# Kernel tuning notes

Measured on AMD Instinct MI355X. Metric: run time of the kernel, lower is better.

Reference implementation:

```python
import jax, jax.numpy as jnp
import numpy as np

B, S, E, H = 2, 2048, 1024, 16
D = E // H  # head_dim = 64

def setup_inputs() -> dict:
    key = jax.random.key(0)
    ks = jax.random.split(key, 9)
    scale = 1.0 / np.sqrt(E)
    inp = {"x": jax.random.normal(ks[0], (B, S, E), dtype=jnp.float32)}
    for i, name in enumerate(["q", "k", "v", "o"]):
        inp[f"W{name}"] = jax.random.uniform(ks[1 + 2 * i], (E, E), jnp.float32, -scale, scale)
        inp[f"b{name}"] = jax.random.uniform(ks[2 + 2 * i], (E,), jnp.float32, -scale, scale)
    return inp

def reference(x, Wq, bq, Wk, bk, Wv, bv, Wo, bo):
    b, s, e = x.shape
    q = x @ Wq + bq
    k = x @ Wk + bk
    v = x @ Wv + bv
    # Faithful to source: view(B, H, S, D) with NO transpose -> splits the
    # sequence dimension across heads (each head sees a contiguous chunk of
    # s*d elements reinterpreted as [s, d]).
    q = q.reshape(b, H, s, D)
    k = k.reshape(b, H, s, D)
    v = v.reshape(b, H, s, D)
    scores = jnp.einsum("bhqd,bhkd->bhqk", q, k) / np.sqrt(D)
    # mask=False in source still adds a zeros mask (no-op); omitted.
    probs = jax.nn.softmax(scores, axis=-1)
    xhat = jnp.einsum("bhqk,bhkd->bhqd", probs, v)
    # transpose(1, 2).contiguous().view(B, S, E)
    xhat = xhat.transpose(0, 2, 1, 3).reshape(b, s, e)
    return xhat @ Wo + bo
```

## Files before the change

kernel.cpp:

```cpp
#include <hip/hip_runtime.h>
#include <math.h>

#define B_ 2
#define S_ 2048
#define E_ 1024
#define H_ 16
#define D_ 64

typedef __attribute__((ext_vector_type(8))) short short8;
typedef __attribute__((ext_vector_type(4))) float f32x4;
typedef __attribute__((ext_vector_type(4))) unsigned short us4;
typedef __attribute__((ext_vector_type(8))) unsigned short us8;
typedef unsigned short ushort_t;

#define MFMA16 __builtin_amdgcn_mfma_f32_16x16x32_bf16

__device__ __forceinline__ ushort_t f2bf(float f) {
    unsigned int u = __float_as_uint(f);
    u += 0x7FFFu + ((u >> 16) & 1u);
    return (ushort_t)(u >> 16);
}
__device__ __forceinline__ float bf2f(ushort_t h) {
    return __uint_as_float((unsigned int)h << 16);
}

__device__ __forceinline__ void gload16(const void* g, void* l) {
    __builtin_amdgcn_global_load_lds(
        (__attribute__((address_space(1))) void*)(unsigned long long)g,
        (__attribute__((address_space(3))) void*)(unsigned int)(unsigned long long)l,
        16, 0, 0);
}

__global__ __launch_bounds__(256)
void split_x(const float* __restrict__ in, ushort_t* __restrict__ hi)
{
    const size_t base = ((size_t)blockIdx.x * 256 + threadIdx.x) * 8;
    float v[8];
    *reinterpret_cast<float4*>(&v[0]) = *reinterpret_cast<const float4*>(&in[base]);
    *reinterpret_cast<float4*>(&v[4]) = *reinterpret_cast<const float4*>(&in[base + 4]);
    us8 h;
#pragma unroll
    for (int j = 0; j < 8; ++j) h[j] = f2bf(v[j]);
    *reinterpret_cast<us8*>(&hi[base]) = h;
}

__global__ __launch_bounds__(256)
void wsplit_t(const float* __restrict__ Wq, const float* __restrict__ Wk,
              const float* __restrict__ Wv, const float* __restrict__ Wo,
              ushort_t* __restrict__ Wth, ushort_t* __restrict__ Wtl)
{
    __shared__ float T[64][65];
    const int tid = threadIdx.x;
    const int z = blockIdx.z;
    const float* W = (z == 0) ? Wq : (z == 1) ? Wk : (z == 2) ? Wv : Wo;
    const int kt = blockIdx.y * 64;
    const int nt = blockIdx.x * 64;

    const int lr = (tid >> 4) * 4;
    const int lc = (tid & 15) * 4;
#pragma unroll
    for (int i = 0; i < 4; ++i) {
        float4 v = *reinterpret_cast<const float4*>(&W[(size_t)(kt + lr + i) * 1024 + nt + lc]);
        T[lr + i][lc + 0] = v.x; T[lr + i][lc + 1] = v.y;
        T[lr + i][lc + 2] = v.z; T[lr + i][lc + 3] = v.w;
    }
    __syncthreads();

    const int n = tid >> 2;
    const int kc = (tid & 3) * 16;
    us8 h[2], l[2];
#pragma unroll
    for (int u = 0; u < 2; ++u)
#pragma unroll
        for (int j = 0; j < 8; ++j) {
            float v = T[kc + u * 8 + j][n];
            ushort_t hh = f2bf(v);
            h[u][j] = hh;
            l[u][j] = f2bf(v - bf2f(hh));
        }
    ushort_t* dh = Wth + ((size_t)z * 1024 + nt + n) * 1024 + kt + kc;
    ushort_t* dl = Wtl + ((size_t)z * 1024 + nt + n) * 1024 + kt + kc;
    *reinterpret_cast<us8*>(dh)     = h[0];
    *reinterpret_cast<us8*>(dh + 8) = h[1];
    *reinterpret_cast<us8*>(dl)     = l[0];
    *reinterpret_cast<us8*>(dl + 8) = l[1];
}

__global__ __launch_bounds__(256, 3)
void gemm_qkv(const ushort_t* __restrict__ xh, const ushort_t* __restrict__ Wth,
              const float* __restrict__ bq, const float* __restrict__ bk,
              const float* __restrict__ bv,
              ushort_t* __restrict__ Qb, ushort_t* __restrict__ Kb,
              ushort_t* __restrict__ Vb, float qalpha)
{
    __shared__ ushort_t As[128 * 32], Bs[128 * 32];
    const int which = blockIdx.x >> 3;
    const int n0 = (blockIdx.x & 7) * 128;
    const int m0 = blockIdx.y * 128;
    const ushort_t* Bh = Wth + (size_t)which * 1024 * 1024;
    const float* bias = (which == 0) ? bq : (which == 1) ? bk : bv;
    ushort_t* out = (which == 0) ? Qb : (which == 1) ? Kb : Vb;
    const float alpha = (which == 0) ? qalpha : 1.0f;

    const int tid  = threadIdx.x;
    const int lane = tid & 63;
    const int w    = tid >> 6;
    const int l15  = lane & 15;
    const int g    = lane >> 4;
    const int wr   = w >> 1;
    const int wc   = w & 1;

    const int sr  = lane >> 2;
    const int scz = (lane & 3) ^ ((sr >> 1) & 3);
    const int sc  = scz * 8;
    const int j0 = w * 2, j1 = j0 + 1;

    const ushort_t* gA0 = xh + (size_t)(m0 + j0 * 16 + sr) * 1024 + sc;
    const ushort_t* gA1 = xh + (size_t)(m0 + j1 * 16 + sr) * 1024 + sc;
    const ushort_t* gB0 = Bh + (size_t)(n0 + j0 * 16 + sr) * 1024 + sc;
    const ushort_t* gB1 = Bh + (size_t)(n0 + j1 * 16 + sr) * 1024 + sc;

    const int sx  = (l15 >> 1) & 3;
    const int rd1 = (((g >> 1) + 0) ^ sx) * 8 + (g & 1) * 4;
    const int rd2 = (((g >> 1) + 2) ^ sx) * 8 + (g & 1) * 4;

    f32x4 acc[4][4];
#pragma unroll
    for (int i = 0; i < 4; ++i)
#pragma unroll
        for (int j = 0; j < 4; ++j) { acc[i][j][0] = 0.f; acc[i][j][1] = 0.f; acc[i][j][2] = 0.f; acc[i][j][3] = 0.f; }

    for (int kt = 0; kt < 32; ++kt) {
        const int k0 = kt * 32;
        if (kt) __syncthreads();
        gload16(gA0 + k0, As + j0 * 512);
        gload16(gA1 + k0, As + j1 * 512);
        gload16(gB0 + k0, Bs + j0 * 512);
        gload16(gB1 + k0, Bs + j1 * 512);
        asm volatile("s_waitcnt vmcnt(0)" ::: "memory");
        __syncthreads();

        short8 bh[4];
#pragma unroll
        for (int nb = 0; nb < 4; ++nb) {
            const int rb = (wc * 64 + nb * 16 + l15) * 32;
            union { us4 h[2]; short8 s; } u;
            u.h[0] = *reinterpret_cast<const us4*>(Bs + rb + rd1);
            u.h[1] = *reinterpret_cast<const us4*>(Bs + rb + rd2);
            bh[nb] = u.s;
        }
#pragma unroll
        for (int mb = 0; mb < 4; ++mb) {
            const int rb = (wr * 64 + mb * 16 + l15) * 32;
            union { us4 h[2]; short8 s; } ua;
            ua.h[0] = *reinterpret_cast<const us4*>(As + rb + rd1);
            ua.h[1] = *reinterpret_cast<const us4*>(As + rb + rd2);
            const short8 ah = ua.s;
#pragma unroll
            for (int nb = 0; nb < 4; ++nb)
                acc[mb][nb] = MFMA16(ah, bh[nb], acc[mb][nb], 0, 0, 0);
        }
    }

    float bvv[4];
#pragma unroll
    for (int nb = 0; nb < 4; ++nb) bvv[nb] = bias[n0 + wc * 64 + nb * 16 + l15];
#pragma unroll
    for (int mb = 0; mb < 4; ++mb)
#pragma unroll
        for (int r = 0; r < 4; ++r) {
            const size_t row = m0 + wr * 64 + mb * 16 + 4 * g + r;
#pragma unroll
            for (int nb = 0; nb < 4; ++nb) {
                const float vv = (acc[mb][nb][r] + bvv[nb]) * alpha;
                out[row * 1024 + n0 + wc * 64 + nb * 16 + l15] = f2bf(vv);
            }
        }
}

__global__ __launch_bounds__(256, 2)
void gemm_o64(const ushort_t* __restrict__ Ah, const ushort_t* __restrict__ Al,
              const ushort_t* __restrict__ Bh, const ushort_t* __restrict__ Bl,
              const float* __restrict__ bias, float* __restrict__ out)
{
    __shared__ ushort_t AsH[128 * 32], AsL[128 * 32], BsH[64 * 32], BsL[64 * 32];
    const int tid  = threadIdx.x;
    const int lane = tid & 63;
    const int w    = tid >> 6;
    const int l15  = lane & 15;
    const int g    = lane >> 4;
    const int wr   = w >> 1;
    const int wc   = w & 1;
    const int n0 = blockIdx.x * 64;
    const int m0 = blockIdx.y * 128;

    const int sr  = lane >> 2;
    const int scz = (lane & 3) ^ ((sr >> 1) & 3);
    const int sc  = scz * 8;
    const int ja0 = 2 * w, ja1 = 2 * w + 1;

    const ushort_t* gAh0 = Ah + (size_t)(m0 + ja0 * 16 + sr) * 1024 + sc;
    const ushort_t* gAh1 = Ah + (size_t)(m0 + ja1 * 16 + sr) * 1024 + sc;
    const ushort_t* gAl0 = Al + (size_t)(m0 + ja0 * 16 + sr) * 1024 + sc;
    const ushort_t* gAl1 = Al + (size_t)(m0 + ja1 * 16 + sr) * 1024 + sc;
    const ushort_t* gBh0 = Bh + (size_t)(n0 + w * 16 + sr) * 1024 + sc;
    const ushort_t* gBl0 = Bl + (size_t)(n0 + w * 16 + sr) * 1024 + sc;

    const int sx  = (l15 >> 1) & 3;
    const int rd1 = (((g >> 1) + 0) ^ sx) * 8 + (g & 1) * 4;
    const int rd2 = (((g >> 1) + 2) ^ sx) * 8 + (g & 1) * 4;

    f32x4 acc[4][2];
#pragma unroll
    for (int i = 0; i < 4; ++i)
#pragma unroll
        for (int j = 0; j < 2; ++j) { acc[i][j][0] = 0.f; acc[i][j][1] = 0.f; acc[i][j][2] = 0.f; acc[i][j][3] = 0.f; }

    for (int kt = 0; kt < 32; ++kt) {
        const int k0 = kt * 32;
        if (kt) __syncthreads();
        gload16(gAh0 + k0, AsH + ja0 * 512);
        gload16(gAh1 + k0, AsH + ja1 * 512);
        gload16(gAl0 + k0, AsL + ja0 * 512);
        gload16(gAl1 + k0, AsL + ja1 * 512);
        gload16(gBh0 + k0, BsH + w * 512);
        gload16(gBl0 + k0, BsL + w * 512);
        asm volatile("s_waitcnt vmcnt(0)" ::: "memory");
        __syncthreads();

        short8 bh[2], bl[2];
#pragma unroll
        for (int nb = 0; nb < 2; ++nb) {
            const int rb = (wc * 32 + nb * 16 + l15) * 32;
            union { us4 h[2]; short8 s; } u;
            u.h[0] = *reinterpret_cast<const us4*>(BsH + rb + rd1);
            u.h[1] = *reinterpret_cast<const us4*>(BsH + rb + rd2);
            bh[nb] = u.s;
            union { us4 h[2]; short8 s; } v;
            v.h[0] = *reinterpret_cast<const us4*>(BsL + rb + rd1);
            v.h[1] = *reinterpret_cast<const us4*>(BsL + rb + rd2);
            bl[nb] = v.s;
        }
#pragma unroll
        for (int mb = 0; mb < 4; ++mb) {
            const int rb = (wr * 64 + mb * 16 + l15) * 32;
            union { us4 h[2]; short8 s; } ua;
            ua.h[0] = *reinterpret_cast<const us4*>(AsH + rb + rd1);
            ua.h[1] = *reinterpret_cast<const us4*>(AsH + rb + rd2);
            union { us4 h[2]; short8 s; } ul;
            ul.h[0] = *reinterpret_cast<const us4*>(AsL + rb + rd1);
            ul.h[1] = *reinterpret_cast<const us4*>(AsL + rb + rd2);
            const short8 ah = ua.s, al = ul.s;
#pragma unroll
            for (int nb = 0; nb < 2; ++nb) {
                acc[mb][nb] = MFMA16(ah, bh[nb], acc[mb][nb], 0, 0, 0);
                acc[mb][nb] = MFMA16(al, bh[nb], acc[mb][nb], 0, 0, 0);
                acc[mb][nb] = MFMA16(ah, bl[nb], acc[mb][nb], 0, 0, 0);
            }
        }
    }

    float bvv[2];
#pragma unroll
    for (int nb = 0; nb < 2; ++nb) bvv[nb] = bias[n0 + wc * 32 + nb * 16 + l15];
#pragma unroll
    for (int mb = 0; mb < 4; ++mb)
#pragma unroll
        for (int r = 0; r < 4; ++r) {
            const size_t row = m0 + wr * 64 + mb * 16 + 4 * g + r;
#pragma unroll
            for (int nb = 0; nb < 2; ++nb)
                out[row * 1024 + n0 + wc * 32 + nb * 16 + l15] = acc[mb][nb][r] + bvv[nb];
        }
}

__global__ __launch_bounds__(256, 2)
void attn_mfma(const ushort_t* __restrict__ Q, const ushort_t* __restrict__ K,
               const ushort_t* __restrict__ V, ushort_t* __restrict__ XHh,
               ushort_t* __restrict__ XHl)
{
    __shared__ __align__(16) ushort_t Kf[4 * 2 * 64 * 8];
    __shared__ __align__(16) ushort_t Vf[4 * 2 * 64 * 8];

    const int tid  = threadIdx.x;
    const int w    = tid >> 6;
    const int lane = tid & 63;
    const int l15  = lane & 15;
    const int g    = lane >> 4;

    const int qb = blockIdx.x;
    const int bh = blockIdx.y;
    const int b  = bh >> 4;
    const int hh = bh & 15;
    const size_t hoff = (size_t)b * S_ * E_ + (size_t)hh * S_ * D_;
    const ushort_t* Qh = Q + hoff;
    const ushort_t* Kh = K + hoff;
    const ushort_t* Vh = V + hoff;

    const int qw = qb * 128 + w * 32;

    short8 qf[2][2];
#pragma unroll
    for (int qg = 0; qg < 2; ++qg)
#pragma unroll
        for (int m = 0; m < 2; ++m) {
            const ushort_t* src = &Qh[(size_t)(qw + 16 * qg + l15) * D_ + 32 * m + 4 * g];
            us4 lo = *reinterpret_cast<const us4*>(src);
            us4 hi = *reinterpret_cast<const us4*>(src + 16);
            union { us4 h[2]; short8 s; } u;
            u.h[0] = lo; u.h[1] = hi;
            qf[qg][m] = u.s;
        }

    const int kr  = tid >> 2;
    const int kc0 = tid & 3;
    const int kkc = tid >> 4;
    const int vdc = tid & 15;
    const int vmc = kkc >> 3;
    const int vh  = (kkc >> 2) & 1;
    const int vg  = kkc & 3;
    const int vn  = vdc >> 2;

    f32x4 o[2][4];
#pragma unroll
    for (int qg = 0; qg < 2; ++qg)
#pragma unroll
        for (int n = 0; n < 4; ++n)
#pragma unroll
            for (int r = 0; r < 4; ++r) o[qg][n][r] = 0.f;

    float mrun[2] = {-1e30f, -1e30f};
    float lrun[2] = {0.f, 0.f};

    for (int kt = 0; kt < S_ / 64; ++kt) {
        us8 kreg[2];
#pragma unroll
        for (int u = 0; u < 2; ++u) {
            const int c8 = kc0 + 4 * u;
            kreg[u] = *reinterpret_cast<const us8*>(&Kh[(size_t)(kt * 64 + kr) * D_ + 8 * c8]);
        }
        us4 vreg[4];
#pragma unroll
        for (int i = 0; i < 4; ++i)
            vreg[i] = *reinterpret_cast<const us4*>(&Vh[(size_t)(kt * 64 + 4 * kkc + i) * D_ + 4 * vdc]);

        __syncthreads();

#pragma unroll
        for (int u = 0; u < 2; ++u) {
            const int c8 = kc0 + 4 * u;
            const int m = c8 >> 2;
            const int h = (c8 >> 1) & 1;
#pragma unroll
            for (int jh = 0; jh < 2; ++jh) {
                const int gk = (2 * c8 + jh) & 3;
                const int slot = gk * 16 + (kr & 15);
                us4 val;
#pragma unroll
                for (int i = 0; i < 4; ++i) val[i] = (ushort_t)kreg[u][4 * jh + i];
                *reinterpret_cast<us4*>(&Kf[((((kr >> 4) * 2 + m) * 64 + slot) * 8) + h * 4]) = val;
            }
        }
#pragma unroll
        for (int jj = 0; jj < 4; ++jj) {
            us4 val;
#pragma unroll
            for (int i = 0; i < 4; ++i) val[i] = vreg[i][jj];
            const int slot = vg * 16 + 4 * (vdc & 3) + jj;
            *reinterpret_cast<us4*>(&Vf[(((vn * 2 + vmc) * 64 + slot) * 8) + vh * 4]) = val;
        }
        __syncthreads();

        short8 kf[4][2];
#pragma unroll
        for (int kkb = 0; kkb < 4; ++kkb)
#pragma unroll
            for (int m = 0; m < 2; ++m)
                kf[kkb][m] = *reinterpret_cast<const short8*>(&Kf[((kkb * 2 + m) * 64 + lane) * 8]);

        f32x4 s[2][4];
#pragma unroll
        for (int qg = 0; qg < 2; ++qg)
#pragma unroll
            for (int kkb = 0; kkb < 4; ++kkb) {
                f32x4 z; z[0] = 0.f; z[1] = 0.f; z[2] = 0.f; z[3] = 0.f;
                z = MFMA16(kf[kkb][0], qf[qg][0], z, 0, 0, 0);
                s[qg][kkb] = MFMA16(kf[kkb][1], qf[qg][1], z, 0, 0, 0);
            }

        short8 vf[4][2];
#pragma unroll
        for (int n = 0; n < 4; ++n)
#pragma unroll
            for (int m = 0; m < 2; ++m)
                vf[n][m] = *reinterpret_cast<const short8*>(&Vf[((n * 2 + m) * 64 + lane) * 8]);

#pragma unroll
        for (int qg = 0; qg < 2; ++qg) {
            float t = s[qg][0][0];
#pragma unroll
            for (int kkb = 0; kkb < 4; ++kkb)
#pragma unroll
                for (int r = 0; r < 4; ++r) t = fmaxf(t, s[qg][kkb][r]);
            t = fmaxf(t, __shfl_xor(t, 16));
            t = fmaxf(t, __shfl_xor(t, 32));
            const float mnew = fmaxf(mrun[qg], t);
            const float corr = __builtin_amdgcn_exp2f(mrun[qg] - mnew);

            float rs = 0.f;
#pragma unroll
            for (int kkb = 0; kkb < 4; ++kkb)
#pragma unroll
                for (int r = 0; r < 4; ++r) {
                    const float p = __builtin_amdgcn_exp2f(s[qg][kkb][r] - mnew);
                    s[qg][kkb][r] = p;
                    rs += p;
                }
            rs += __shfl_xor(rs, 16);
            rs += __shfl_xor(rs, 32);
            lrun[qg] = lrun[qg] * corr + rs;
            mrun[qg] = mnew;

#pragma unroll
            for (int r = 0; r < 4; ++r) {
                const float c4 = __shfl(corr, 4 * g + r);
#pragma unroll
                for (int n = 0; n < 4; ++n) o[qg][n][r] *= c4;
            }

            short8 pa[2];
#pragma unroll
            for (int m = 0; m < 2; ++m) {
                us8 tmp;
#pragma unroll
                for (int r = 0; r < 4; ++r) {
                    tmp[r]     = f2bf(s[qg][2 * m][r]);
                    tmp[r + 4] = f2bf(s[qg][2 * m + 1][r]);
                }
                union { us8 u8; short8 s8; } cvt; cvt.u8 = tmp;
                pa[m] = cvt.s8;
            }
#pragma unroll
            for (int n = 0; n < 4; ++n) {
                o[qg][n] = MFMA16(pa[0], vf[n][0], o[qg][n], 0, 0, 0);
                o[qg][n] = MFMA16(pa[1], vf[n][1], o[qg][n], 0, 0, 0);
            }
        }
    }

#pragma unroll
    for (int qg = 0; qg < 2; ++qg) {
        const float invl = 1.f / lrun[qg];
#pragma unroll
        for (int r = 0; r < 4; ++r) {
            const float iv = __shfl(invl, 4 * g + r);
            const int row = qw + 16 * qg + 4 * g + r;
            const size_t base = ((size_t)b * S_ + row) * E_ + hh * D_ + l15;
#pragma unroll
            for (int n = 0; n < 4; ++n) {
                const float vv = o[qg][n][r] * iv;
                const ushort_t hi = f2bf(vv);
                XHh[base + 16 * n] = hi;
                XHl[base + 16 * n] = f2bf(vv - bf2f(hi));
            }
        }
    }
}

extern "C" void kernel_launch(void* const* d_in, const int* in_sizes, int n_in,
                              void* d_out, int out_size, void* d_ws, size_t ws_size,
                              hipStream_t stream) {
    (void)in_sizes; (void)n_in; (void)out_size; (void)ws_size;
    const float* x  = (const float*)d_in[0];
    const float* Wq = (const float*)d_in[1];
    const float* bq = (const float*)d_in[2];
    const float* Wk = (const float*)d_in[3];
    const float* bk = (const float*)d_in[4];
    const float* Wv = (const float*)d_in[5];
    const float* bv = (const float*)d_in[6];
    const float* Wo = (const float*)d_in[7];
    const float* bo = (const float*)d_in[8];
    float* out = (float*)d_out;

    char* ws = (char*)d_ws;
    const size_t MB8 = 8ull * 1024 * 1024;
    ushort_t* xhi = (ushort_t*)(ws);
    ushort_t* XHl = (ushort_t*)(ws + MB8);
    ushort_t* Wth = (ushort_t*)(ws + 2 * MB8);
    ushort_t* Wtl = (ushort_t*)(ws + 3 * MB8);
    ushort_t* Qb  = (ushort_t*)(ws + 4 * MB8);
    ushort_t* Kb  = (ushort_t*)(ws + 5 * MB8);
    ushort_t* Vb  = (ushort_t*)(ws + 6 * MB8);
    ushort_t* XHh = xhi;

    const float qalpha = 0.125f * 1.4426950408889634f;

    split_x<<<dim3(2048), dim3(256), 0, stream>>>(x, xhi);
    wsplit_t<<<dim3(16, 16, 4), dim3(256), 0, stream>>>(Wq, Wk, Wv, Wo, Wth, Wtl);

    gemm_qkv<<<dim3(24, 32), dim3(256), 0, stream>>>(xhi, Wth,
                                                     bq, bk, bv, Qb, Kb, Vb, qalpha);

    attn_mfma<<<dim3(16, 32), dim3(256), 0, stream>>>(Qb, Kb, Vb, XHh, XHl);

    gemm_o64<<<dim3(16, 32), dim3(256), 0, stream>>>(XHh, XHl,
                                                     Wth + 3ull * 1024 * 1024,
                                                     Wtl + 3ull * 1024 * 1024,
                                                     bo, out);
}
```

Before: 166.3 us.

## Halve attention query rows per warp and double the grid for occupancy

Measured after the change: 174.3 us. +4.8%, slower.

```diff
diff --git a/kernel.cpp b/kernel.cpp
--- a/kernel.cpp
+++ b/kernel.cpp
@@ -1,4 +1,5 @@
 #include <hip/hip_runtime.h>
+#include <hip/hip_bf16.h>
 #include <math.h>
 
 #define B_ 2
@@ -22,6 +23,10 @@
 }
 __device__ __forceinline__ float bf2f(ushort_t h) {
     return __uint_as_float((unsigned int)h << 16);
+}
+__device__ __forceinline__ ushort_t f2bf_fast(float f) {
+    __hip_bfloat16 h = __float2bfloat16(f);
+    return *reinterpret_cast<ushort_t*>(&h);
 }
 
 __device__ __forceinline__ void gload16(const void* g, void* l) {
@@ -274,7 +279,7 @@
         }
 }
 
-__global__ __launch_bounds__(256, 2)
+__global__ __launch_bounds__(256, 4)
 void attn_mfma(const ushort_t* __restrict__ Q, const ushort_t* __restrict__ K,
                const ushort_t* __restrict__ V, ushort_t* __restrict__ XHh,
                ushort_t* __restrict__ XHl)
@@ -297,20 +302,18 @@
     const ushort_t* Kh = K + hoff;
     const ushort_t* Vh = V + hoff;
 
-    const int qw = qb * 128 + w * 32;
-
-    short8 qf[2][2];
-#pragma unroll
-    for (int qg = 0; qg < 2; ++qg)
-#pragma unroll
-        for (int m = 0; m < 2; ++m) {
-            const ushort_t* src = &Qh[(size_t)(qw + 16 * qg + l15) * D_ + 32 * m + 4 * g];
-            us4 lo = *reinterpret_cast<const us4*>(src);
-            us4 hi = *reinterpret_cast<const us4*>(src + 16);
-            union { us4 h[2]; short8 s; } u;
-            u.h[0] = lo; u.h[1] = hi;
-            qf[qg][m] = u.s;
-        }
+    const int qw = qb * 64 + w * 16;
+
+    short8 qf[2];
+#pragma unroll
+    for (int m = 0; m < 2; ++m) {
+        const ushort_t* src = &Qh[(size_t)(qw + l15) * D_ + 32 * m + 4 * g];
+        us4 lo = *reinterpret_cast<const us4*>(src);
+        us4 hi = *reinterpret_cast<const us4*>(src + 16);
+        union { us4 h[2]; short8 s; } u;
+        u.h[0] = lo; u.h[1] = hi;
+        qf[m] = u.s;
+    }
 
     const int kr  = tid >> 2;
     const int kc0 = tid & 3;
@@ -321,16 +324,14 @@
     const int vg  = kkc & 3;
     const int vn  = vdc >> 2;
 
-    f32x4 o[2][4];
-#pragma unroll
-    for (int qg = 0; qg < 2; ++qg)
-#pragma unroll
-        for (int n = 0; n < 4; ++n)
-#pragma unroll
-            for (int r = 0; r < 4; ++r) o[qg][n][r] = 0.f;
-
-    float mrun[2] = {-1e30f, -1e30f};
-    float lrun[2] = {0.f, 0.f};
+    f32x4 o[4];
+#pragma unroll
+    for (int n = 0; n < 4; ++n)
+#pragma unroll
+        for (int r = 0; r < 4; ++r) o[n][r] = 0.f;
+
+    float mrun = -1e30f;
+    float lrun = 0.f;
 
     for (int kt = 0; kt < S_ / 64; ++kt) {
         us8 kreg[2];
@@ -378,15 +379,13 @@
             for (int m = 0; m < 2; ++m)
                 kf[kkb][m] = *reinterpret_cast<const short8*>(&Kf[((kkb * 2 + m) * 64 + lane) * 8]);
 
-        f32x4 s[2][4];
-#pragma unroll
-        for (int qg = 0; qg < 2; ++qg)
-#pragma unroll
-            for (int kkb = 0; kkb < 4; ++kkb) {
-                f32x4 z; z[0] = 0.f; z[1] = 0.f; z[2] = 0.f; z[3] = 0.f;
-                z = MFMA16(kf[kkb][0], qf[qg][0], z, 0, 0, 0);
-                s[qg][kkb] = MFMA16(kf[kkb][1], qf[qg][1], z, 0, 0, 0);
-            }
+        f32x4 s[4];
+#pragma unroll
+        for (int kkb = 0; kkb < 4; ++kkb) {
+            f32x4 z; z[0] = 0.f; z[1] = 0.f; z[2] = 0.f; z[3] = 0.f;
+            z = MFMA16(kf[kkb][0], qf[0], z, 0, 0, 0);
+            s[kkb] = MFMA16(kf[kkb][1], qf[1], z, 0, 0, 0);
+        }
 
         short8 vf[4][2];
 #pragma unroll
@@ -395,74 +394,68 @@
             for (int m = 0; m < 2; ++m)
                 vf[n][m] = *reinterpret_cast<const short8*>(&Vf[((n * 2 + m) * 64 + lane) * 8]);
 
-#pragma unroll
-        for (int qg = 0; qg < 2; ++qg) {
-            float t = s[qg][0][0];
-#pragma unroll
-            for (int kkb = 0; kkb < 4; ++kkb)
-#pragma unroll
-                for (int r = 0; r < 4; ++r) t = fmaxf(t, s[qg][kkb][r]);
-            t = fmaxf(t, __shfl_xor(t, 16));
-            t = fmaxf(t, __shfl_xor(t, 32));
-            const float mnew = fmaxf(mrun[qg], t);
-            const float corr = __builtin_amdgcn_exp2f(mrun[qg] - mnew);
-
-            float rs = 0.f;
-#pragma unroll
-            for (int kkb = 0; kkb < 4; ++kkb)
-#pragma unroll
-                for (int r = 0; r < 4; ++r) {
-                    const float p = __builtin_amdgcn_exp2f(s[qg][kkb][r] - mnew);
-                    s[qg][kkb][r] = p;
-                    rs += p;
-                }
-            rs += __shfl_xor(rs, 16);
-            rs += __shfl_xor(rs, 32);
-            lrun[qg] = lrun[qg] * corr + rs;
-            mrun[qg] = mnew;
-
+        float t = s[0][0];
+#pragma unroll
+        for (int kkb = 0; kkb < 4; ++kkb)
+#pragma unroll
+            for (int r = 0; r < 4; ++r) t = fmaxf(t, s[kkb][r]);
+        t = fmaxf(t, __shfl_xor(t, 16));
+        t = fmaxf(t, __shfl_xor(t, 32));
+        const float mnew = fmaxf(mrun, t);
+        const float corr = __builtin_amdgcn_exp2f(mrun - mnew);
+
+        float rs = 0.f;
+#pragma unroll
+        for (int kkb = 0; kkb < 4; ++kkb)
 #pragma unroll
             for (int r = 0; r < 4; ++r) {
-                const float c4 = __shfl(corr, 4 * g + r);
-#pragma unroll
-                for (int n = 0; n < 4; ++n) o[qg][n][r] *= c4;
+                const float p = __builtin_amdgcn_exp2f(s[kkb][r] - mnew);
+                s[kkb][r] = p;
+                rs += p;
             }
-
-            short8 pa[2];
-#pragma unroll
-            for (int m = 0; m < 2; ++m) {
-                us8 tmp;
-#pragma unroll
-                for (int r = 0; r < 4; ++r) {
-                    tmp[r]     = f2bf(s[qg][2 * m][r]);
-                    tmp[r + 4] = f2bf(s[qg][2 * m + 1][r]);
-                }
-                union { us8 u8; short8 s8; } cvt; cvt.u8 = tmp;
-                pa[m] = cvt.s8;
+        rs += __shfl_xor(rs, 16);
+        rs += __shfl_xor(rs, 32);
+        lrun = lrun * corr + rs;
+        mrun = mnew;
+
+#pragma unroll
+        for (int r = 0; r < 4; ++r) {
+            const float c4 = __shfl(corr, 4 * g + r);
+#pragma unroll
+            for (int n = 0; n < 4; ++n) o[n][r] *= c4;
+        }
+
+        short8 pa[2];
+#pragma unroll
+        for (int m = 0; m < 2; ++m) {
+            us8 tmp;
+#pragma unroll
+            for (int r = 0; r < 4; ++r) {
+                tmp[r]     = f2bf_fast(s[2 * m][r]);
+                tmp[r + 4] = f2bf_fast(s[2 * m + 1][r]);
             }
-#pragma unroll
-            for (int n = 0; n < 4; ++n) {
-                o[qg][n] = MFMA16(pa[0], vf[n][0], o[qg][n], 0, 0, 0);
-                o[qg][n] = MFMA16(pa[1], vf[n][1], o[qg][n], 0, 0, 0);
-            }
+            union { us8 u8; short8 s8; } cvt; cvt.u8 = tmp;
+            pa[m] = cvt.s8;
+        }
+#pragma unroll
+        for (int n = 0; n < 4; ++n) {
+            o[n] = MFMA16(pa[0], vf[n][0], o[n], 0, 0, 0);
+            o[n] = MFMA16(pa[1], vf[n][1], o[n], 0, 0, 0);
         }
     }
 
-#pragma unroll
-    for (int qg = 0; qg < 2; ++qg) {
-        const float invl = 1.f / lrun[qg];
-#pragma unroll
-        for (int r = 0; r < 4; ++r) {
-            const float iv = __shfl(invl, 4 * g + r);
-            const int row = qw + 16 * qg + 4 * g + r;
-            const size_t base = ((size_t)b * S_ + row) * E_ + hh * D_ + l15;
-#pragma unroll
-            for (int n = 0; n < 4; ++n) {
-                const float vv = o[qg][n][r] * iv;
-                const ushort_t hi = f2bf(vv);
-                XHh[base + 16 * n] = hi;
-                XHl[base + 16 * n] = f2bf(vv - bf2f(hi));
-            }
+    const float invl = 1.f / lrun;
+#pragma unroll
+    for (int r = 0; r < 4; ++r) {
+        const float iv = __shfl(invl, 4 * g + r);
+        const int row = qw + 4 * g + r;
+        const size_t base = ((size_t)b * S_ + row) * E_ + hh * D_ + l15;
+#pragma unroll
+        for (int n = 0; n < 4; ++n) {
+            const float vv = o[n][r] * iv;
+            const ushort_t hi = f2bf(vv);
+            XHh[base + 16 * n] = hi;
+            XHl[base + 16 * n] = f2bf(vv - bf2f(hi));
         }
     }
 }
@@ -501,7 +494,7 @@
     gemm_qkv<<<dim3(24, 32), dim3(256), 0, stream>>>(xhi, Wth,
                                                      bq, bk, bv, Qb, Kb, Vb, qalpha);
 
-    attn_mfma<<<dim3(16, 32), dim3(256), 0, stream>>>(Qb, Kb, Vb, XHh, XHl);
+    attn_mfma<<<dim3(32, 32), dim3(256), 0, stream>>>(Qb, Kb, Vb, XHh, XHl);
 
     gemm_o64<<<dim3(16, 32), dim3(256), 0, stream>>>(XHh, XHl,
                                                      Wth + 3ull * 1024 * 1024,
```
